# Kernel tuning notes

Measured on AMD Instinct MI355X. Metric: run time of the kernel, lower is better.

Reference implementation:

```python
import jax, jax.numpy as jnp
import numpy as np

N_HEADS = 16

def setup_inputs() -> dict:
    key = jax.random.key(0)
    k1, k2, k3 = jax.random.split(key, 3)
    B, T, C = 2, 2048, 1024
    x = jax.random.normal(k1, (B, T, C), dtype=jnp.float32)
    w_attn = jax.random.normal(k2, (3 * C, C), dtype=jnp.float32) * (C ** -0.5)
    b_attn = jnp.zeros((3 * C,), dtype=jnp.float32)
    w_proj = jax.random.normal(k3, (C, C), dtype=jnp.float32) * (C ** -0.5)
    b_proj = jnp.zeros((C,), dtype=jnp.float32)
    return {"x": x, "w_attn": w_attn, "b_attn": b_attn, "w_proj": w_proj, "b_proj": b_proj}

def reference(x, w_attn, b_attn, w_proj, b_proj):
    B, T, C = x.shape
    H = N_HEADS
    Dh = C // H
    qkv = x @ w_attn.T + b_attn                      # [B,T,3C]
    q, k, v = jnp.split(qkv, 3, axis=-1)             # each [B,T,C]
    q = q.reshape(B, T, H, Dh).transpose(0, 2, 1, 3)  # [B,H,T,Dh]
    k = k.reshape(B, T, H, Dh).transpose(0, 2, 1, 3)
    v = v.reshape(B, T, H, Dh).transpose(0, 2, 1, 3)
    scores = jnp.einsum('bhqd,bhkd->bhqk', q, k) * (Dh ** -0.5)  # [B,H,T,T]
    causal = jnp.tril(jnp.ones((T, T), dtype=bool))
    scores = jnp.where(causal, scores, jnp.float32(-jnp.inf))
    probs = jax.nn.softmax(scores, axis=-1)
    out = jnp.einsum('bhqk,bhkd->bhqd', probs, v)    # [B,H,T,Dh]
    out = out.transpose(0, 2, 1, 3).reshape(B, T, C)
    out = out @ w_proj.T + b_proj
    return out
```

## Files before the change

kernel.cpp:

```cpp
#include <hip/hip_runtime.h>
#include <math.h>

#define GB 2
#define GT_SEQ 2048
#define GC 1024
#define GH 16
#define GDH 64
#define GM (GB * GT_SEQ)

typedef __attribute__((ext_vector_type(8))) short bf16x8;
typedef __attribute__((ext_vector_type(8))) unsigned short u16x8;
typedef __attribute__((ext_vector_type(4))) unsigned short u16x4;
typedef __attribute__((ext_vector_type(4))) float f32x4;
typedef unsigned int u32;

#define QSCALE 0.18033688f

__device__ __forceinline__ unsigned short f2bf(float f) {
    unsigned int u = __float_as_uint(f);
    u += 0x7FFFu + ((u >> 16) & 1u);
    return (unsigned short)(u >> 16);
}
__device__ __forceinline__ float bf2f(unsigned short u) {
    return __uint_as_float(((unsigned int)u) << 16);
}
__device__ __forceinline__ float hw_exp2(float x) {
    return __builtin_amdgcn_exp2f(x);
}
__device__ __forceinline__ u32 pack2bf(float lo, float hi) {
    return ((u32)f2bf(hi) << 16) | (u32)f2bf(lo);
}

#define GLOAD_LDS16(g, l) __builtin_amdgcn_global_load_lds( \
    (const __attribute__((address_space(1))) void*)(g),      \
    (__attribute__((address_space(3))) void*)(l), 16, 0, 0)

__device__ __forceinline__ bf16x8 frag_ld(const char* base, int r, int kch) {
    return *reinterpret_cast<const bf16x8*>(base + r * 128 + ((kch ^ (r & 7)) << 4));
}

__global__ __launch_bounds__(256) void cast3_f32_bf16(
    const float* __restrict__ a, unsigned short* __restrict__ oa, int na,
    const float* __restrict__ b, unsigned short* __restrict__ ob, int nb,
    const float* __restrict__ c, unsigned short* __restrict__ oc)
{
    const int i = (blockIdx.x * 256 + threadIdx.x) * 4;
    const float* src; unsigned short* dst; int off;
    if (i < na)            { src = a; dst = oa; off = i; }
    else if (i < na + nb)  { src = b; dst = ob; off = i - na; }
    else                   { src = c; dst = oc; off = i - na - nb; }
    const float4 v = *reinterpret_cast<const float4*>(&src[off]);
    ushort4 o;
    o.x = f2bf(v.x); o.y = f2bf(v.y); o.z = f2bf(v.z); o.w = f2bf(v.w);
    *reinterpret_cast<ushort4*>(&dst[off]) = o;
}

__global__ __launch_bounds__(256) void gemm_mfma_bt(
    const unsigned short* __restrict__ A,
    const unsigned short* __restrict__ B,
    const float* __restrict__ bias,
    float* __restrict__ Cf,
    unsigned short* __restrict__ Cb,
    int M, int N, int K)
{
    __shared__ char As[128 * 128];
    __shared__ char Bs[128 * 128];

    const int tid  = threadIdx.x;
    const int lane = tid & 63;
    const int w    = tid >> 6;
    const int wm   = w >> 1;
    const int wn   = w & 1;
    const int m0 = blockIdx.y * 128;
    const int n0 = blockIdx.x * 128;

    f32x4 acc[4][4];
#pragma unroll
    for (int i = 0; i < 4; ++i)
#pragma unroll
        for (int j = 0; j < 4; ++j) acc[i][j] = (f32x4){0.f, 0.f, 0.f, 0.f};

    const int wbase = (tid & ~63);

    for (int k0 = 0; k0 < K; k0 += 64) {
        const char* Ag = (const char*)(A + (size_t)m0 * K + k0);
        const char* Bg = (const char*)(B + (size_t)n0 * K + k0);
#pragma unroll
        for (int i = 0; i < 4; ++i) {
            const int c = i * 256 + tid;
            const int row = c >> 3, cin = c & 7;
            const size_t goff = (size_t)row * (K * 2) + (size_t)((cin ^ (row & 7)) << 4);
            GLOAD_LDS16(Ag + goff, As + (i * 256 + wbase) * 16);
            GLOAD_LDS16(Bg + goff, Bs + (i * 256 + wbase) * 16);
        }
        __syncthreads();

#pragma unroll
        for (int ks = 0; ks < 2; ++ks) {
            const int kch = ks * 4 + (lane >> 4);
            bf16x8 a[4], b[4];
#pragma unroll
            for (int mi = 0; mi < 4; ++mi)
                a[mi] = frag_ld(As, wm * 64 + mi * 16 + (lane & 15), kch);
#pragma unroll
            for (int ni = 0; ni < 4; ++ni)
                b[ni] = frag_ld(Bs, wn * 64 + ni * 16 + (lane & 15), kch);
#pragma unroll
            for (int mi = 0; mi < 4; ++mi)
#pragma unroll
                for (int ni = 0; ni < 4; ++ni)
                    acc[mi][ni] = __builtin_amdgcn_mfma_f32_16x16x32_bf16(
                        a[mi], b[ni], acc[mi][ni], 0, 0, 0);
        }
        __syncthreads();
    }

    const int lc  = lane & 15;
    const int lr4 = (lane >> 4) * 4;
#pragma unroll
    for (int ni = 0; ni < 4; ++ni) {
        const int gcol = n0 + wn * 64 + ni * 16 + lc;
        const float bv = bias[gcol];
#pragma unroll
        for (int mi = 0; mi < 4; ++mi) {
            const int grow0 = m0 + wm * 64 + mi * 16 + lr4;
#pragma unroll
            for (int j = 0; j < 4; ++j) {
                const float v = acc[mi][ni][j] + bv;
                if (Cb) Cb[(size_t)(grow0 + j) * N + gcol] = f2bf(v);
                else    Cf[(size_t)(grow0 + j) * N + gcol] = v;
            }
        }
    }
}

__global__ __launch_bounds__(256) void transpose_v(
    const unsigned short* __restrict__ qkvb, unsigned short* __restrict__ Vt)
{
    __shared__ unsigned short vt[64][72];
    const int tid = threadIdx.x;
    const int t0  = blockIdx.x * 64;
    const int bh  = blockIdx.y;
    const int b = bh >> 4, h = bh & 15;
    const unsigned short* src = qkvb + (size_t)(b * GT_SEQ) * (3 * GC) + 2 * GC + h * GDH;
    unsigned short* dstb = Vt + (size_t)bh * GDH * GT_SEQ;

#pragma unroll
    for (int i = 0; i < 2; ++i) {
        const int c = i * 256 + tid;
        const int tr = c >> 3, ch = c & 7;
        *reinterpret_cast<u16x8*>(&vt[tr][ch * 8]) =
            *reinterpret_cast<const u16x8*>(src + (size_t)(t0 + tr) * (3 * GC) + ch * 8);
    }
    __syncthreads();
#pragma unroll
    for (int i = 0; i < 2; ++i) {
        const int c = i * 256 + tid;
        const int d = c >> 3, ch = c & 7;
        u16x8 o;
#pragma unroll
        for (int e = 0; e < 8; ++e) o[e] = vt[ch * 8 + e][d];
        *reinterpret_cast<u16x8*>(dstb + (size_t)d * GT_SEQ + t0 + ch * 8) = o;
    }
}

__global__ __launch_bounds__(256) void flash_attn_mfma9(
    const unsigned short* __restrict__ qkvb,
    const unsigned short* __restrict__ Vt,
    unsigned short* __restrict__ O)
{
    __shared__ __align__(16) char Ks[2][64 * 128];
    __shared__ __align__(16) char Vs[2][64 * 128];

    const int tid  = threadIdx.x;
    const int lane = tid & 63;
    const int w    = tid >> 6;
    const int l15  = lane & 15;
    const int l4   = lane >> 4;
    const int bid  = blockIdx.x;
    const int xcd  = bid & 7;
    const int rest = bid >> 3;
    const int bh   = xcd * 4 + (rest & 3);
    const int qb   = 31 - (rest >> 2);
    const int b    = bh >> 4, h = bh & 15;
    const int q0w  = qb * 64 + w * 16;

    const unsigned short* hQ = qkvb + (size_t)(b * GT_SEQ) * (3 * GC) + h * GDH;
    const char* hKc = (const char*)(qkvb + (size_t)(b * GT_SEQ) * (3 * GC) + GC + h * GDH);
    const char* hVc = (const char*)(Vt + (size_t)bh * GDH * GT_SEQ);

    bf16x8 qf[2];
#pragma unroll
    for (int s = 0; s < 2; ++s) {
        bf16x8 v = *reinterpret_cast<const bf16x8*>(
            hQ + (size_t)(q0w + l15) * (3 * GC) + s * 32 + l4 * 8);
#pragma unroll
        for (int e = 0; e < 8; ++e)
            v[e] = (short)f2bf(bf2f((unsigned short)v[e]) * QSCALE);
        qf[s] = v;
    }

    f32x4 acc_o[4];
    float l_part = 0.f;
    float m_r = -1e30f;
#pragma unroll
    for (int nd = 0; nd < 4; ++nd) acc_o[nd] = (f32x4){0.f, 0.f, 0.f, 0.f};

    const int nt = qb + 1;
    const int wbase16 = (tid & ~63) * 16;

    auto STAGE = [&](int bb, int t) {
        const int k0 = t * 64;
#pragma unroll
        for (int i = 0; i < 2; ++i) {
            const int c = i * 256 + tid;
            const int row = c >> 3, cin = c & 7;
            GLOAD_LDS16(hKc + (size_t)(k0 + row) * (3 * GC * 2) + ((cin ^ (row & 7)) << 4),
                        Ks[bb] + i * 4096 + wbase16);
            GLOAD_LDS16(hVc + (size_t)row * 4096 + (size_t)k0 * 2 + ((cin ^ (row & 7)) << 4),
                        Vs[bb] + i * 4096 + wbase16);
        }
    };

    STAGE(0, 0);
    __syncthreads();

    for (int t = 0; t < nt; ++t) {
        if (t + 1 < nt) STAGE((t + 1) & 1, t + 1);

        const int k0 = t * 64;
        const char* Kb = Ks[t & 1];
        const char* Vb = Vs[t & 1];

        if (k0 <= q0w + 15) {
            f32x4 s_acc[4];
#pragma unroll
            for (int ni = 0; ni < 4; ++ni) s_acc[ni] = (f32x4){0.f, 0.f, 0.f, 0.f};
#pragma unroll
            for (int s = 0; s < 2; ++s) {
                bf16x8 kf[4];
#pragma unroll
                for (int ni = 0; ni < 4; ++ni)
                    kf[ni] = frag_ld(Kb, ni * 16 + l15, s * 4 + l4);
#pragma unroll
                for (int ni = 0; ni < 4; ++ni)
                    s_acc[ni] = __builtin_amdgcn_mfma_f32_16x16x32_bf16(
                        kf[ni], qf[s], s_acc[ni], 0, 0, 0);
            }

            if (k0 + 63 > q0w) {
#pragma unroll
                for (int ni = 0; ni < 4; ++ni)
#pragma unroll
                    for (int j = 0; j < 4; ++j)
                        if (k0 + ni * 16 + l4 * 4 + j > q0w + l15)
                            s_acc[ni][j] = -1e30f;
            }

            float r = fmaxf(fmaxf(s_acc[0][0], s_acc[0][1]),
                            fmaxf(s_acc[0][2], s_acc[0][3]));
#pragma unroll
            for (int ni = 1; ni < 4; ++ni)
                r = fmaxf(r, fmaxf(fmaxf(s_acc[ni][0], s_acc[ni][1]),
                                   fmaxf(s_acc[ni][2], s_acc[ni][3])));
            const int ok = (r <= m_r + 8.f) ? 1 : 0;
            if (!__all(ok)) {
                r = fmaxf(r, __shfl_xor(r, 16));
                r = fmaxf(r, __shfl_xor(r, 32));
                const float mnew = fmaxf(m_r, r);
                const float corr = hw_exp2(m_r - mnew);
                m_r = mnew;
                l_part *= corr;
#pragma unroll
                for (int nd = 0; nd < 4; ++nd) acc_o[nd] *= corr;
            }

#pragma unroll
            for (int s = 0; s < 2; ++s) {
                union { u32 w4[4]; bf16x8 v; } pw;
                {
                    f32x4 pa, pb;
#pragma unroll
                    for (int j = 0; j < 4; ++j) {
                        pa[j] = hw_exp2(s_acc[2 * s + 0][j] - m_r);
                        pb[j] = hw_exp2(s_acc[2 * s + 1][j] - m_r);
                    }
                    l_part += (pa[0] + pa[1]) + (pa[2] + pa[3])
                            + (pb[0] + pb[1]) + (pb[2] + pb[3]);
                    pw.w4[0] = pack2bf(pa[0], pa[1]);
                    pw.w4[1] = pack2bf(pa[2], pa[3]);
                    pw.w4[2] = pack2bf(pb[0], pb[1]);
                    pw.w4[3] = pack2bf(pb[2], pb[3]);
                }
                const int ch0 = s * 4 + (l4 >> 1);
                const int sub = (l4 & 1) * 8;
#pragma unroll
                for (int nd = 0; nd < 4; ++nd) {
                    const int d  = nd * 16 + l15;
                    const char* vrow = Vb + d * 128;
                    union { u16x4 h2[2]; bf16x8 v; } vbs;
                    vbs.h2[0] = *reinterpret_cast<const u16x4*>(
                        vrow + ((ch0 ^ (d & 7)) << 4) + sub);
                    vbs.h2[1] = *reinterpret_cast<const u16x4*>(
                        vrow + (((ch0 + 2) ^ (d & 7)) << 4) + sub);
                    acc_o[nd] = __builtin_amdgcn_mfma_f32_16x16x32_bf16(
                        vbs.v, pw.v, acc_o[nd], 0, 0, 0);
                }
            }
        }

        __syncthreads();
    }

    {
        float lp = l_part;
        lp += __shfl_xor(lp, 16);
        lp += __shfl_xor(lp, 32);
        const float inv = 1.f / lp;
        const int q = q0w + l15;
        const size_t rbase = (size_t)(b * GT_SEQ + q) * GC + h * GDH;
#pragma unroll
        for (int nd = 0; nd < 4; ++nd) {
            ushort4 ov;
            ov.x = f2bf(acc_o[nd][0] * inv);
            ov.y = f2bf(acc_o[nd][1] * inv);
            ov.z = f2bf(acc_o[nd][2] * inv);
            ov.w = f2bf(acc_o[nd][3] * inv);
            *reinterpret_cast<ushort4*>(&O[rbase + nd * 16 + l4 * 4]) = ov;
        }
    }
}

extern "C" void kernel_launch(void* const* d_in, const int* in_sizes, int n_in,
                              void* d_out, int out_size, void* d_ws, size_t ws_size,
                              hipStream_t stream) {
    (void)in_sizes; (void)n_in; (void)out_size; (void)ws_size;
    const float* x      = (const float*)d_in[0];
    const float* w_attn = (const float*)d_in[1];
    const float* b_attn = (const float*)d_in[2];
    const float* w_proj = (const float*)d_in[3];
    const float* b_proj = (const float*)d_in[4];
    float* out = (float*)d_out;

    unsigned short* xb   = (unsigned short*)d_ws;
    unsigned short* wab  = xb   + (size_t)GM * GC;
    unsigned short* wpb  = wab  + (size_t)3 * GC * GC;
    unsigned short* qkvb = wpb  + (size_t)GC * GC;
    unsigned short* Vt   = qkvb + (size_t)GM * 3 * GC;
    unsigned short* aob  = xb;

    cast3_f32_bf16<<<dim3(8192), dim3(256), 0, stream>>>(
        x, xb, GM * GC, w_attn, wab, 3 * GC * GC, w_proj, wpb);

    gemm_mfma_bt<<<dim3(3 * GC / 128, GM / 128), dim3(256), 0, stream>>>(
        xb, wab, b_attn, nullptr, qkvb, GM, 3 * GC, GC);

    transpose_v<<<dim3(GT_SEQ / 64, GB * GH), dim3(256), 0, stream>>>(qkvb, Vt);

    flash_attn_mfma9<<<dim3(1024), dim3(256), 0, stream>>>(qkvb, Vt, aob);

    gemm_mfma_bt<<<dim3(GC / 128, GM / 128), dim3(256), 0, stream>>>(
        aob, wpb, b_proj, out, nullptr, GM, GC, GC);
}
```

Measured before the change: 118.3 us.

## Compute softmax row sums via MFMA, use hardware bf16 pack, swizzle GEMM tiles across XCDs

The attention kernel now gets the softmax denominator from an extra MFMA that multiplies a ones matrix by the bf16 probability tile. This replaces the scalar adds and cross-lane shuffles, and the sum now uses the bf16-rounded probabilities, matching what is fed to the PV product. Probability packing switches to the library float2-to-bfloat162 conversion, which may map to a packed convert instruction. The GEMM remaps block IDs so that consecutive blocks on the same XCD cover neighbouring tiles, aiming for better L2 reuse, at the cost of one extra MFMA per step in attention.

```diff
diff --git a/kernel.cpp b/kernel.cpp
--- a/kernel.cpp
+++ b/kernel.cpp
@@ -1,4 +1,5 @@
 #include <hip/hip_runtime.h>
+#include <hip/hip_bf16.h>
 #include <math.h>
 
 #define GB 2
@@ -27,8 +28,9 @@
 __device__ __forceinline__ float hw_exp2(float x) {
     return __builtin_amdgcn_exp2f(x);
 }
-__device__ __forceinline__ u32 pack2bf(float lo, float hi) {
-    return ((u32)f2bf(hi) << 16) | (u32)f2bf(lo);
+__device__ __forceinline__ u32 pk_bf16(float lo, float hi) {
+    __hip_bfloat162 h = __float22bfloat162_rn(make_float2(lo, hi));
+    return *reinterpret_cast<u32*>(&h);
 }
 
 #define GLOAD_LDS16(g, l) __builtin_amdgcn_global_load_lds( \
@@ -71,8 +73,14 @@
     const int w    = tid >> 6;
     const int wm   = w >> 1;
     const int wn   = w & 1;
-    const int m0 = blockIdx.y * 128;
-    const int n0 = blockIdx.x * 128;
+
+    const int gx  = gridDim.x;
+    const int lid = blockIdx.y * gx + blockIdx.x;
+    const int nwg = gx * gridDim.y;
+    const int cpx = nwg >> 3;
+    const int swz = (lid & 7) * cpx + (lid >> 3);
+    const int m0 = (swz / gx) * 128;
+    const int n0 = (swz % gx) * 128;
 
     f32x4 acc[4][4];
 #pragma unroll
@@ -189,6 +197,10 @@
     const char* hKc = (const char*)(qkvb + (size_t)(b * GT_SEQ) * (3 * GC) + GC + h * GDH);
     const char* hVc = (const char*)(Vt + (size_t)bh * GDH * GT_SEQ);
 
+    bf16x8 ones_a;
+#pragma unroll
+    for (int e = 0; e < 8; ++e) ones_a[e] = (short)0x3F80;
+
     bf16x8 qf[2];
 #pragma unroll
     for (int s = 0; s < 2; ++s) {
@@ -201,7 +213,7 @@
     }
 
     f32x4 acc_o[4];
-    float l_part = 0.f;
+    f32x4 acc_l = (f32x4){0.f, 0.f, 0.f, 0.f};
     float m_r = -1e30f;
 #pragma unroll
     for (int nd = 0; nd < 4; ++nd) acc_o[nd] = (f32x4){0.f, 0.f, 0.f, 0.f};
@@ -270,7 +282,7 @@
                 const float mnew = fmaxf(m_r, r);
                 const float corr = hw_exp2(m_r - mnew);
                 m_r = mnew;
-                l_part *= corr;
+                acc_l *= corr;
 #pragma unroll
                 for (int nd = 0; nd < 4; ++nd) acc_o[nd] *= corr;
             }
@@ -285,13 +297,13 @@
                         pa[j] = hw_exp2(s_acc[2 * s + 0][j] - m_r);
                         pb[j] = hw_exp2(s_acc[2 * s + 1][j] - m_r);
                     }
-                    l_part += (pa[0] + pa[1]) + (pa[2] + pa[3])
-                            + (pb[0] + pb[1]) + (pb[2] + pb[3]);
-                    pw.w4[0] = pack2bf(pa[0], pa[1]);
-                    pw.w4[1] = pack2bf(pa[2], pa[3]);
-                    pw.w4[2] = pack2bf(pb[0], pb[1]);
-                    pw.w4[3] = pack2bf(pb[2], pb[3]);
+                    pw.w4[0] = pk_bf16(pa[0], pa[1]);
+                    pw.w4[1] = pk_bf16(pa[2], pa[3]);
+                    pw.w4[2] = pk_bf16(pb[0], pb[1]);
+                    pw.w4[3] = pk_bf16(pb[2], pb[3]);
                 }
+                acc_l = __builtin_amdgcn_mfma_f32_16x16x32_bf16(
+                    ones_a, pw.v, acc_l, 0, 0, 0);
                 const int ch0 = s * 4 + (l4 >> 1);
                 const int sub = (l4 & 1) * 8;
 #pragma unroll
@@ -313,10 +325,7 @@
     }
 
     {
-        float lp = l_part;
-        lp += __shfl_xor(lp, 16);
-        lp += __shfl_xor(lp, 32);
-        const float inv = 1.f / lp;
+        const float inv = 1.f / acc_l[0];
         const int q = q0w + l15;
         const size_t rbase = (size_t)(b * GT_SEQ + q) * GC + h * GDH;
 #pragma unroll
```

After: 116.3 us. Within noise of the previous version (-1.7%).
